# Kernel tuning notes

Hardware: AMD Instinct MI355X
Metric: run time of the kernel (lower is better)

Reference implementation:

```python
import jax, jax.numpy as jnp
import numpy as np
import math

B, L, H, NH = 4, 2048, 2048, 16
HD = H // NH  # head_dim = 128
ROPE_BASE = 10000.0


def rotate_half(x):
    x1, x2 = jnp.split(x, 2, axis=-1)
    return jnp.concatenate((-x2, x1), axis=-1)


def rope_cos_sin(seq_len, dim, dtype=jnp.float32):
    inv_freq = 1.0 / (ROPE_BASE ** (jnp.arange(0, dim, 2, dtype=jnp.float32) / dim))
    t = jnp.arange(seq_len, dtype=jnp.float32)
    freqs = jnp.outer(t, inv_freq)              # [L, dim/2]
    emb = jnp.concatenate((freqs, freqs), -1)   # [L, dim]
    return jnp.cos(emb).astype(dtype), jnp.sin(emb).astype(dtype)


def setup_inputs() -> dict:
    key = jax.random.key(0)
    ks = jax.random.split(key, 5)
    x = jax.random.normal(ks[0], (B, L, H), dtype=jnp.float32)
    # causal mask, broadcastable over [B, NH, L, L]; 0 -> masked
    mask = jnp.tril(jnp.ones((L, L), dtype=jnp.int32))[None, None]
    s = 0.02
    Wq = jax.random.normal(ks[1], (H, H), dtype=jnp.float32) * s
    Wk = jax.random.normal(ks[2], (H, H), dtype=jnp.float32) * s
    Wv = jax.random.normal(ks[3], (H, H), dtype=jnp.float32) * s
    Wo = jax.random.normal(ks[4], (H, H), dtype=jnp.float32) * s
    return {"x": x, "mask": mask, "Wq": Wq, "Wk": Wk, "Wv": Wv, "Wo": Wo}


def reference(x, mask, Wq, Wk, Wv, Wo):
    b, l, _ = x.shape
    # nn.Linear: y = x @ W.T (weight shape [out, in])
    q = (x @ Wq.T).reshape(b, l, NH, HD).transpose(0, 2, 1, 3)  # [B,H,L,D]
    k = (x @ Wk.T).reshape(b, l, NH, HD).transpose(0, 2, 1, 3)
    v = (x @ Wv.T).reshape(b, l, NH, HD).transpose(0, 2, 1, 3)
    cos, sin = rope_cos_sin(l, HD, x.dtype)  # [L, D] broadcasts over [B,H,L,D]
    q = q * cos + rotate_half(q) * sin
    k = k * cos + rotate_half(k) * sin
    attn = jnp.einsum("bhqd,bhkd->bhqk", q, k) / math.sqrt(HD)
    attn = jnp.where(mask == 0, jnp.float32(-jnp.inf), attn)
    attn = jax.nn.softmax(attn.astype(jnp.float32), axis=-1).astype(x.dtype)
    out = jnp.einsum("bhqk,bhkd->bhqd", attn, v)
    out = out.transpose(0, 2, 1, 3).reshape(b, l, NH * HD)
    return out @ Wo.T
```

## Files before the change

### kernel.cpp

```cpp
#include <hip/hip_runtime.h>
#include <cstdint>
#include <cmath>

#define B_   4
#define L_   2048
#define H_   2048
#define NH_  16
#define HD_  128
#define ML_  (B_*L_)

using short8 = __attribute__((ext_vector_type(8))) short;
using f32x4  = __attribute__((ext_vector_type(4))) float;
using f32x16 = __attribute__((ext_vector_type(16))) float;
using uint4v = __attribute__((ext_vector_type(4))) unsigned;

__device__ inline short f2bf(float f){
  unsigned u = __builtin_bit_cast(unsigned, f);
  unsigned r = u + 0x7FFFu + ((u >> 16) & 1u);
  return (short)(r >> 16);
}
__device__ inline float bf2f(short s){
  unsigned u = ((unsigned)(unsigned short)s) << 16;
  return __builtin_bit_cast(float, u);
}

#define GLD16(gp, lp) __builtin_amdgcn_global_load_lds(                      \
    (const __attribute__((address_space(1))) void*)(gp),                     \
    (__attribute__((address_space(3))) void*)(lp), 16, 0, 0)

__device__ inline unsigned cvtpk_bf16(float lo, float hi){
  unsigned d;
  asm("v_cvt_pk_bf16_f32 %0, %1, %2" : "=v"(d) : "v"(lo), "v"(hi));
  return d;
}
__device__ inline void permswap32(unsigned &a, unsigned &b){
  asm volatile("v_permlane32_swap_b32 %0, %1" : "+v"(a), "+v"(b));
}
__device__ inline float cross_half_max(float x){
  return fmaxf(x, __shfl_xor(x, 32));
}
__device__ inline float cross_half_add(float x){
  return x + __shfl_xor(x, 32);
}

__global__ void rope_table(float* __restrict__ cosT, float* __restrict__ sinT){
  int idx = blockIdx.x * 256 + threadIdx.x;
  if (idx >= L_ * 64) return;
  int l = idx >> 6, d = idx & 63;
  float invf = powf(10000.0f, -(float)d * (1.0f/64.0f));
  float fr = (float)l * invf;
  cosT[idx] = cosf(fr);
  sinT[idx] = sinf(fr);
}

__global__ __launch_bounds__(256)
void cvt_bf16(const float* __restrict__ in, short* __restrict__ out, int n8){
  int i = blockIdx.x * 256 + threadIdx.x;
  if (i >= n8) return;
  const float4* p = (const float4*)(in + (size_t)i * 8);
  float4 a = p[0], b = p[1];
  short8 s;
  s[0]=f2bf(a.x); s[1]=f2bf(a.y); s[2]=f2bf(a.z); s[3]=f2bf(a.w);
  s[4]=f2bf(b.x); s[5]=f2bf(b.y); s[6]=f2bf(b.z); s[7]=f2bf(b.w);
  *(short8*)(out + (size_t)i * 8) = s;
}

__global__ __launch_bounds__(256)
void cvt_w3(const float* __restrict__ W0, const float* __restrict__ W1,
            const float* __restrict__ W2, short* __restrict__ out){
  int i = blockIdx.x * 256 + threadIdx.x;
  const int per = H_ * H_ / 8;
  const float* src; int j;
  if (i < per)            { src = W0; j = i; }
  else if (i < 2 * per)   { src = W1; j = i - per; }
  else                    { src = W2; j = i - 2 * per; }
  const float4* p = (const float4*)(src + (size_t)j * 8);
  float4 a = p[0], b = p[1];
  short8 s;
  s[0]=f2bf(a.x); s[1]=f2bf(a.y); s[2]=f2bf(a.z); s[3]=f2bf(a.w);
  s[4]=f2bf(b.x); s[5]=f2bf(b.y); s[6]=f2bf(b.z); s[7]=f2bf(b.w);
  *(short8*)(out + (size_t)i * 8) = s;
}

template<int QKV, int OUT_F32>
__global__ __launch_bounds__(512, 2)
void gemm256_bt(const short* __restrict__ A, const short* __restrict__ Bw,
                void* __restrict__ C0, void* __restrict__ C1,
                void* __restrict__ C2)
{
  constexpr int K = 2048, N = 2048;
  __shared__ short sA[4][256 * 32];
  __shared__ short sB[4][256 * 32];
  const int tid  = threadIdx.x;
  const int lane = tid & 63;
  const int wave = tid >> 6;
  const int wr = wave >> 2, wc = wave & 3;
  const int ln = lane & 15, g = lane >> 4;

  const int blk = blockIdx.x;
  int n_t, m_t;
  if constexpr (QKV) { int i = blk >> 3; n_t = (blk & 7) + 8 * (i >> 5); m_t = i & 31; }
  else               { n_t = blk & 7;    m_t = blk >> 3; }
  const int m0 = m_t * 256;
  const int nb0 = n_t * 256;

  const int u0 = wave * 64 + lane;
  const int u1 = u0 + 512;
  const int r0 = u0 >> 2, c0 = (((u0 & 3) ^ (r0 & 3) ^ ((r0 >> 2) & 3))) * 8;
  const int r1 = u1 >> 2, c1 = (((u1 & 3) ^ (r1 & 3) ^ ((r1 >> 2) & 3))) * 8;

  f32x4 acc[8][4];
  #pragma unroll
  for (int m = 0; m < 8; m++)
    #pragma unroll
    for (int n = 0; n < 4; n++) acc[m][n] = {0.f, 0.f, 0.f, 0.f};

#define STAGE256(T) do {                                                     \
    const int _b = (T) & 3; const int _k = (T) * 32;                         \
    GLD16(A  + (size_t)(m0 + r0) * K + _k + c0, &sA[_b][wave * 512]);        \
    GLD16(A  + (size_t)(m0 + r1) * K + _k + c1, &sA[_b][4096 + wave * 512]); \
    GLD16(Bw + (size_t)(nb0 + r0) * K + _k + c0, &sB[_b][wave * 512]);       \
    GLD16(Bw + (size_t)(nb0 + r1) * K + _k + c1, &sB[_b][4096 + wave * 512]);\
  } while (0)

#define TILE256(T, VMN, PF) do {                                             \
    asm volatile("s_waitcnt vmcnt(" #VMN ")" ::: "memory");                  \
    __builtin_amdgcn_s_barrier();                                            \
    asm volatile("" ::: "memory");                                           \
    const short* _at = &sA[(T) & 3][0];                                      \
    const short* _bt = &sB[(T) & 3][0];                                      \
    short8 af[8], bfr[4];                                                    \
    const int _sl = (g ^ (ln & 3) ^ ((ln >> 2) & 3)) * 8;                    \
    _Pragma("unroll")                                                        \
    for (int m = 0; m < 8; m++)                                              \
      af[m] = *(const short8*)(_at + (wr * 128 + m * 16 + ln) * 32 + _sl);   \
    _Pragma("unroll")                                                        \
    for (int n = 0; n < 4; n++)                                              \
      bfr[n] = *(const short8*)(_bt + (wc * 64 + n * 16 + ln) * 32 + _sl);   \
    if (PF) STAGE256((T) + 3);                                               \
    __builtin_amdgcn_s_setprio(1);                                           \
    _Pragma("unroll")                                                        \
    for (int m = 0; m < 8; m++)                                              \
      _Pragma("unroll")                                                      \
      for (int n = 0; n < 4; n++)                                            \
        acc[m][n] = __builtin_amdgcn_mfma_f32_16x16x32_bf16(af[m], bfr[n],   \
                                                            acc[m][n], 0, 0, 0); \
    __builtin_amdgcn_s_setprio(0);                                           \
  } while (0)

  STAGE256(0); STAGE256(1); STAGE256(2);

  for (int t = 0; t < 61; ++t) TILE256(t, 8, true);
  TILE256(61, 8, false);
  TILE256(62, 4, false);
  TILE256(63, 0, false);

#undef STAGE256
#undef TILE256

  void* Cp; int cb;
  if constexpr (QKV) {
    int w = n_t >> 3;
    Cp = (w == 0) ? C0 : (w == 1) ? C1 : C2;
    cb = (n_t & 7) * 256;
  } else { Cp = C0; cb = nb0; }
  #pragma unroll
  for (int m = 0; m < 8; m++)
    #pragma unroll
    for (int n = 0; n < 4; n++)
      #pragma unroll
      for (int r = 0; r < 4; r++) {
        int row = m0 + wr * 128 + m * 16 + g * 4 + r;
        int col = cb + wc * 64 + n * 16 + ln;
        float v = acc[m][n][r];
        if constexpr (OUT_F32) ((float*)Cp)[(size_t)row * N + col] = v;
        else                   ((short*)Cp)[(size_t)row * N + col] = f2bf(v);
      }
}

__global__ __launch_bounds__(256)
void rope_apply_k(short* __restrict__ Kb,
                  const float* __restrict__ cosT, const float* __restrict__ sinT)
{
  int idx = blockIdx.x * 256 + threadIdx.x;
  int row = idx >> 7;
  int rem = idx & 127;
  int h = rem >> 3, ch = rem & 7;
  int l = row & (L_ - 1);
  short* base = Kb + (size_t)row * H_ + h * HD_ + ch * 8;
  short8 lo = *(short8*)base;
  short8 hi = *(short8*)(base + 64);
  const float* cp = cosT + l * 64 + ch * 8;
  const float* sp = sinT + l * 64 + ch * 8;
  short8 nlo, nhi;
  #pragma unroll
  for (int j = 0; j < 8; j++) {
    float c = cp[j], s = sp[j];
    float x0 = bf2f(lo[j]), x1 = bf2f(hi[j]);
    nlo[j] = f2bf(x0 * c - x1 * s);
    nhi[j] = f2bf(x1 * c + x0 * s);
  }
  *(short8*)base        = nlo;
  *(short8*)(base + 64) = nhi;
}

__global__ __launch_bounds__(256)
void transpose_v(const short* __restrict__ Vb, short* __restrict__ VT)
{
  __shared__ short t[64 * 64];
  const int blk = blockIdx.x;
  const int dt = blk & 1, lt = (blk >> 1) & 31, bh = blk >> 6;
  const int b = bh >> 4, h = bh & 15;
  const int l0 = lt * 64, d0 = dt * 64;
  const int tid = threadIdx.x;
  #pragma unroll
  for (int i = 0; i < 2; i++) {
    int u = tid + i * 256;
    int r = u >> 3, c = u & 7;
    short8 v = *(const short8*)(Vb + ((size_t)b * L_ + l0 + r) * H_ + h * HD_ + d0 + c * 8);
    *(short8*)&t[r * 64 + ((c ^ ((r >> 3) & 7)) << 3)] = v;
  }
  __syncthreads();
  #pragma unroll
  for (int i = 0; i < 2; i++) {
    int u = tid + i * 256;
    int d = u >> 3, lc = u & 7;
    short8 o;
    #pragma unroll
    for (int j = 0; j < 8; j++) {
      int l = lc * 8 + j;
      o[j] = t[l * 64 + (((d >> 3) ^ (lc & 7)) << 3) + (d & 7)];
    }
    *(short8*)(VT + ((size_t)bh * HD_ + d0 + d) * L_ + l0 + lc * 8) = o;
  }
}

__global__ __launch_bounds__(512, 2)
void flash_attn(const short* __restrict__ Qb, const short* __restrict__ Kb,
                const short* __restrict__ VT, short* __restrict__ AO,
                const float* __restrict__ cosT, const float* __restrict__ sinT)
{
  __shared__ short lds_k[2][64 * 128];
  __shared__ short lds_v[2][128 * 64];
  __shared__ float f_lds[8][32];

  const int blk = blockIdx.x;
  int bh, j;
  if (blk < 256) { bh = blk & 63; j = 7 - (blk >> 6); }
  else           { int u = blk - 256; bh = u & 63; j = 3 - (u >> 6); }
  const int q0 = j * 256;
  const int T  = 4 * j + 4;
  const int h = bh & 15, b = bh >> 4;
  const int tid = threadIdx.x, wave = tid >> 6, lane = tid & 63;
  const int hi = lane >> 5, l31 = lane & 31;
  const size_t rowbase = (size_t)b * L_;
  const int colbase = h * HD_;
  const short* Kbh  = Kb + rowbase * H_ + colbase;
  const short* VTbh = VT + (size_t)bh * HD_ * L_;
  const int qw = q0 + wave * 32;
  const int qabs = qw + l31;
  const int fsw = (l31 & 7) ^ ((l31 >> 3) & 3);

  short8 qf[8];
  {
    const short* qp = Qb + (rowbase + qabs) * H_ + colbase + hi * 8;
    short8 qraw[8];
    #pragma unroll
    for (int c = 0; c < 8; c++) qraw[c] = *(const short8*)(qp + c * 16);
    const int lq = qabs & (L_ - 1);
    const float* cp = cosT + lq * 64 + hi * 8;
    const float* sp = sinT + lq * 64 + hi * 8;
    #pragma unroll
    for (int c = 0; c < 4; c++) {
      #pragma unroll
      for (int jj = 0; jj < 8; jj++) {
        float cc = cp[c * 16 + jj], ss = sp[c * 16 + jj];
        float lo = bf2f(qraw[c][jj]), hv = bf2f(qraw[c + 4][jj]);
        qf[c][jj]     = f2bf((lo * cc - hv * ss) * 0.08838834764831845f);
        qf[c + 4][jj] = f2bf((hv * cc + lo * ss) * 0.08838834764831845f);
      }
    }
  }

  f32x16 acc_o[4];
  #pragma unroll
  for (int d = 0; d < 4; d++)
    #pragma unroll
    for (int r = 0; r < 16; r++) acc_o[d][r] = 0.f;
  float m_ = -__builtin_inff(), l_ = 0.f;

  auto stage = [&](int k0s, int bufi) {
    #pragma unroll
    for (int i = 0; i < 2; i++) {
      int c = wave * 2 + i;
      {
        int rt = c * 4 + (lane >> 4);
        int cg = (lane & 15) ^ (rt & 7) ^ ((rt >> 3) & 3);
        const short* gp = Kbh + (size_t)(k0s + rt) * H_ + cg * 8;
        GLD16(gp, &lds_k[bufi][c * 512]);
      }
      {
        int rd = c * 8 + (lane >> 3);
        int cg = (lane & 7) ^ (rd & 7) ^ ((rd >> 3) & 3);
        const short* gp = VTbh + (size_t)rd * L_ + k0s + cg * 8;
        GLD16(gp, &lds_v[bufi][c * 512]);
      }
    }
  };

  stage(0, 0);
  __syncthreads();

  for (int t = 0; t < T; ++t) {
    const int k0 = t * 64;
    if (t + 1 < T) stage((t + 1) * 64, (t + 1) & 1);
    const short* kb_ = lds_k[t & 1];
    const short* vb_ = lds_v[t & 1];

    if (k0 <= qw + 31) {
      f32x16 p0, p1;
      #pragma unroll
      for (int r = 0; r < 16; r++) { p0[r] = 0.f; p1[r] = 0.f; }
      __builtin_amdgcn_s_setprio(1);
      #pragma unroll
      for (int c = 0; c < 8; c++) {
        int ch = (c * 2 + hi) ^ fsw;
        short8 kf0 = *(const short8*)(kb_ + l31 * 128 + ch * 8);
        short8 kf1 = *(const short8*)(kb_ + (32 + l31) * 128 + ch * 8);
        p0 = __builtin_amdgcn_mfma_f32_32x32x16_bf16(kf0, qf[c], p0, 0, 0, 0);
        p1 = __builtin_amdgcn_mfma_f32_32x32x16_bf16(kf1, qf[c], p1, 0, 0, 0);
      }
      __builtin_amdgcn_s_setprio(0);

      if (k0 + 63 > qw) {
        #pragma unroll
        for (int r = 0; r < 16; r++) {
          int kvl = (r & 3) + 8 * (r >> 2) + 4 * hi;
          if (k0 + kvl > qabs)      p0[r] = -__builtin_inff();
          if (k0 + 32 + kvl > qabs) p1[r] = -__builtin_inff();
        }
      }

      float mt = p0[0];
      #pragma unroll
      for (int r = 1; r < 16; r++) mt = fmaxf(mt, p0[r]);
      #pragma unroll
      for (int r = 0; r < 16; r++) mt = fmaxf(mt, p1[r]);
      mt = cross_half_max(mt);
      if (!__all(mt <= m_ + 8.0f)) {
        float mnew = fmaxf(m_, mt);
        float f = __expf(m_ - mnew);
        m_ = mnew;
        l_ *= f;
        if (lane < 32) f_lds[wave][lane] = f;
        f32x4 fr[4];
        #pragma unroll
        for (int i = 0; i < 4; i++)
          fr[i] = *(const f32x4*)&f_lds[wave][i * 8 + hi * 4];
        #pragma unroll
        for (int d = 0; d < 4; d++)
          #pragma unroll
          for (int r = 0; r < 16; r++) acc_o[d][r] *= fr[r >> 2][r & 3];
      }
      float ls = 0.f;
      #pragma unroll
      for (int r = 0; r < 16; r++) { p0[r] = __expf(p0[r] - m_); ls += p0[r]; }
      #pragma unroll
      for (int r = 0; r < 16; r++) { p1[r] = __expf(p1[r] - m_); ls += p1[r]; }
      ls = cross_half_add(ls);
      l_ += ls;

      __builtin_amdgcn_s_setprio(1);
      #pragma unroll
      for (int ks = 0; ks < 4; ks++) {
        const f32x16 &pp = (ks < 2) ? p0 : p1;
        const int kk = (ks & 1) * 8;
        unsigned a0 = cvtpk_bf16(pp[kk + 0], pp[kk + 1]);
        unsigned b0 = cvtpk_bf16(pp[kk + 4], pp[kk + 5]);
        permswap32(a0, b0);
        unsigned a1 = cvtpk_bf16(pp[kk + 2], pp[kk + 3]);
        unsigned b1 = cvtpk_bf16(pp[kk + 6], pp[kk + 7]);
        permswap32(a1, b1);
        uint4v w; w[0] = a0; w[1] = a1; w[2] = b0; w[3] = b1;
        short8 af = __builtin_bit_cast(short8, w);
        #pragma unroll
        for (int db = 0; db < 4; db++) {
          int d  = db * 32 + l31;
          int ch = (ks * 2 + hi) ^ fsw;
          short8 vf = *(const short8*)(vb_ + d * 64 + ch * 8);
          acc_o[db] = __builtin_amdgcn_mfma_f32_32x32x16_bf16(af, vf, acc_o[db], 0, 0, 0);
        }
      }
      __builtin_amdgcn_s_setprio(0);
    }
    __syncthreads();
  }

  if (lane < 32) f_lds[wave][lane] = 1.0f / l_;
  f32x4 lr[4];
  #pragma unroll
  for (int i = 0; i < 4; i++)
    lr[i] = *(const f32x4*)&f_lds[wave][i * 8 + hi * 4];
  #pragma unroll
  for (int db = 0; db < 4; db++)
    #pragma unroll
    for (int r = 0; r < 16; r++) {
      int row = qw + (r & 3) + 8 * (r >> 2) + 4 * hi;
      AO[(rowbase + row) * H_ + colbase + db * 32 + l31] =
          f2bf(acc_o[db][r] * lr[r >> 2][r & 3]);
    }
}

extern "C" void kernel_launch(void* const* d_in, const int* in_sizes, int n_in,
                              void* d_out, int out_size, void* d_ws, size_t ws_size,
                              hipStream_t stream)
{
  const float* x  = (const float*)d_in[0];
  const float* Wq = (const float*)d_in[2];
  const float* Wk = (const float*)d_in[3];
  const float* Wv = (const float*)d_in[4];
  const float* Wo = (const float*)d_in[5];
  float* out = (float*)d_out;

  char* ws = (char*)d_ws;
  const size_t SZ = (size_t)ML_ * H_ * sizeof(short);
  short* Qb = (short*)(ws);
  short* Kb = (short*)(ws + SZ);
  short* Vb = (short*)(ws + 2 * SZ);
  short* xb = (short*)(ws + 3 * SZ);
  short* VT = xb;
  short* AO = Vb;
  float* cosT = (float*)(ws + 4 * SZ);
  float* sinT = cosT + (size_t)L_ * 64;
  short* Wb = (short*)(ws + 4 * SZ + (size_t)(1 << 20));
  const size_t NEED_FUSED = 4 * SZ + (1 << 20) + (size_t)3 * H_ * H_ * sizeof(short);
  const bool fused = ws_size >= NEED_FUSED;

  rope_table<<<512, 256, 0, stream>>>(cosT, sinT);

  cvt_bf16<<<ML_ * H_ / 8 / 256, 256, 0, stream>>>(x, xb, ML_ * H_ / 8);

  if (fused) {
    cvt_w3<<<3 * H_ * H_ / 8 / 256, 256, 0, stream>>>(Wq, Wk, Wv, Wb);
    gemm256_bt<1, 0><<<768, 512, 0, stream>>>(xb, Wb, Qb, Kb, Vb);
  } else {
    cvt_bf16<<<H_ * H_ / 8 / 256, 256, 0, stream>>>(Wq, Wb, H_ * H_ / 8);
    gemm256_bt<0, 0><<<256, 512, 0, stream>>>(xb, Wb, Qb, Qb, Qb);
    cvt_bf16<<<H_ * H_ / 8 / 256, 256, 0, stream>>>(Wk, Wb, H_ * H_ / 8);
    gemm256_bt<0, 0><<<256, 512, 0, stream>>>(xb, Wb, Kb, Kb, Kb);
    cvt_bf16<<<H_ * H_ / 8 / 256, 256, 0, stream>>>(Wv, Wb, H_ * H_ / 8);
    gemm256_bt<0, 0><<<256, 512, 0, stream>>>(xb, Wb, Vb, Vb, Vb);
  }

  transpose_v<<<64 * 32 * 2, 256, 0, stream>>>(Vb, VT);

  rope_apply_k<<<ML_ * NH_ * 8 / 256, 256, 0, stream>>>(Kb, cosT, sinT);

  flash_attn<<<512, 512, 0, stream>>>(Qb, Kb, VT, AO, cosT, sinT);

  cvt_bf16<<<H_ * H_ / 8 / 256, 256, 0, stream>>>(Wo, Wb, H_ * H_ / 8);
  gemm256_bt<0, 1><<<256, 512, 0, stream>>>(AO, Wb, out, out, out);
}
```

Baseline: 446.0 us.

## Shrink GEMM tiles to 128x128 and merge prep/post kernels into fewer launches

The GEMM drops from 256x256 tiles with 512 threads to 128x128 tiles with 256 threads. The grid grows from 256 to 1024 blocks per 2048x2048 projection, which gives more parallelism across CUs. The rope table, x/weight conversions and the Wo conversion are merged into one prep kernel, and the V transpose and K rope into one post_qkv kernel, to cut launch count. Smaller tiles reduce operand reuse and raise global/L2 traffic per FLOP.

```diff
diff --git a/kernel.cpp b/kernel.cpp
--- a/kernel.cpp
+++ b/kernel.cpp
@@ -41,6 +41,16 @@
 }
 __device__ inline float cross_half_add(float x){
   return x + __shfl_xor(x, 32);
+}
+
+__device__ inline void cvt8(const float* __restrict__ in, short* __restrict__ out,
+                            int i){
+  const float4* p = (const float4*)(in + (size_t)i * 8);
+  float4 a = p[0], b = p[1];
+  short8 s;
+  s[0]=f2bf(a.x); s[1]=f2bf(a.y); s[2]=f2bf(a.z); s[3]=f2bf(a.w);
+  s[4]=f2bf(b.x); s[5]=f2bf(b.y); s[6]=f2bf(b.z); s[7]=f2bf(b.w);
+  *(short8*)(out + (size_t)i * 8) = s;
 }
 
 __global__ void rope_table(float* __restrict__ cosT, float* __restrict__ sinT){
@@ -57,90 +67,103 @@
 void cvt_bf16(const float* __restrict__ in, short* __restrict__ out, int n8){
   int i = blockIdx.x * 256 + threadIdx.x;
   if (i >= n8) return;
-  const float4* p = (const float4*)(in + (size_t)i * 8);
-  float4 a = p[0], b = p[1];
-  short8 s;
-  s[0]=f2bf(a.x); s[1]=f2bf(a.y); s[2]=f2bf(a.z); s[3]=f2bf(a.w);
-  s[4]=f2bf(b.x); s[5]=f2bf(b.y); s[6]=f2bf(b.z); s[7]=f2bf(b.w);
-  *(short8*)(out + (size_t)i * 8) = s;
+  cvt8(in, out, i);
 }
 
 __global__ __launch_bounds__(256)
-void cvt_w3(const float* __restrict__ W0, const float* __restrict__ W1,
-            const float* __restrict__ W2, short* __restrict__ out){
-  int i = blockIdx.x * 256 + threadIdx.x;
+void prep(const float* __restrict__ x,  const float* __restrict__ Wq,
+          const float* __restrict__ Wk, const float* __restrict__ Wv,
+          const float* __restrict__ Wo, short* __restrict__ xb,
+          short* __restrict__ Wb, short* __restrict__ WoB,
+          float* __restrict__ cosT, float* __restrict__ sinT)
+{
+  const int blk = blockIdx.x, tid = threadIdx.x;
   const int per = H_ * H_ / 8;
-  const float* src; int j;
-  if (i < per)            { src = W0; j = i; }
-  else if (i < 2 * per)   { src = W1; j = i - per; }
-  else                    { src = W2; j = i - 2 * per; }
-  const float4* p = (const float4*)(src + (size_t)j * 8);
-  float4 a = p[0], b = p[1];
-  short8 s;
-  s[0]=f2bf(a.x); s[1]=f2bf(a.y); s[2]=f2bf(a.z); s[3]=f2bf(a.w);
-  s[4]=f2bf(b.x); s[5]=f2bf(b.y); s[6]=f2bf(b.z); s[7]=f2bf(b.w);
-  *(short8*)(out + (size_t)i * 8) = s;
+  if (blk < 8192) {
+    cvt8(x, xb, blk * 256 + tid);
+  } else if (blk < 14336) {
+    int i = (blk - 8192) * 256 + tid;
+    const float* src; int j;
+    if (i < per)          { src = Wq; j = i; }
+    else if (i < 2 * per) { src = Wk; j = i - per; }
+    else                  { src = Wv; j = i - 2 * per; }
+    const float4* p = (const float4*)(src + (size_t)j * 8);
+    float4 a = p[0], b = p[1];
+    short8 s;
+    s[0]=f2bf(a.x); s[1]=f2bf(a.y); s[2]=f2bf(a.z); s[3]=f2bf(a.w);
+    s[4]=f2bf(b.x); s[5]=f2bf(b.y); s[6]=f2bf(b.z); s[7]=f2bf(b.w);
+    *(short8*)(Wb + (size_t)i * 8) = s;
+  } else if (blk < 16384) {
+    cvt8(Wo, WoB, (blk - 14336) * 256 + tid);
+  } else {
+    int idx = (blk - 16384) * 256 + tid;
+    int l = idx >> 6, d = idx & 63;
+    float invf = powf(10000.0f, -(float)d * (1.0f/64.0f));
+    float fr = (float)l * invf;
+    cosT[idx] = cosf(fr);
+    sinT[idx] = sinf(fr);
+  }
 }
 
 template<int QKV, int OUT_F32>
-__global__ __launch_bounds__(512, 2)
-void gemm256_bt(const short* __restrict__ A, const short* __restrict__ Bw,
+__global__ __launch_bounds__(256, 2)
+void gemm128_bt(const short* __restrict__ A, const short* __restrict__ Bw,
                 void* __restrict__ C0, void* __restrict__ C1,
                 void* __restrict__ C2)
 {
   constexpr int K = 2048, N = 2048;
-  __shared__ short sA[4][256 * 32];
-  __shared__ short sB[4][256 * 32];
+  __shared__ short sA[4][128 * 32];
+  __shared__ short sB[4][128 * 32];
   const int tid  = threadIdx.x;
   const int lane = tid & 63;
   const int wave = tid >> 6;
-  const int wr = wave >> 2, wc = wave & 3;
+  const int wr = wave >> 1, wc = wave & 1;
   const int ln = lane & 15, g = lane >> 4;
 
   const int blk = blockIdx.x;
-  int n_t, m_t;
-  if constexpr (QKV) { int i = blk >> 3; n_t = (blk & 7) + 8 * (i >> 5); m_t = i & 31; }
-  else               { n_t = blk & 7;    m_t = blk >> 3; }
-  const int m0 = m_t * 256;
-  const int nb0 = n_t * 256;
-
-  const int u0 = wave * 64 + lane;
-  const int u1 = u0 + 512;
+  const int i = blk >> 3;
+  const int n_t = (blk & 7) + 8 * (i >> 6);
+  const int m_t = i & 63;
+  const int m0 = m_t * 128;
+  const int nb0 = n_t * 128;
+
+  const int u0 = tid;
+  const int u1 = tid + 256;
   const int r0 = u0 >> 2, c0 = (((u0 & 3) ^ (r0 & 3) ^ ((r0 >> 2) & 3))) * 8;
   const int r1 = u1 >> 2, c1 = (((u1 & 3) ^ (r1 & 3) ^ ((r1 >> 2) & 3))) * 8;
 
-  f32x4 acc[8][4];
+  f32x4 acc[4][4];
   #pragma unroll
-  for (int m = 0; m < 8; m++)
+  for (int m = 0; m < 4; m++)
     #pragma unroll
     for (int n = 0; n < 4; n++) acc[m][n] = {0.f, 0.f, 0.f, 0.f};
 
-#define STAGE256(T) do {                                                     \
+#define STAGE128(T) do {                                                     \
     const int _b = (T) & 3; const int _k = (T) * 32;                         \
     GLD16(A  + (size_t)(m0 + r0) * K + _k + c0, &sA[_b][wave * 512]);        \
-    GLD16(A  + (size_t)(m0 + r1) * K + _k + c1, &sA[_b][4096 + wave * 512]); \
+    GLD16(A  + (size_t)(m0 + r1) * K + _k + c1, &sA[_b][2048 + wave * 512]); \
     GLD16(Bw + (size_t)(nb0 + r0) * K + _k + c0, &sB[_b][wave * 512]);       \
-    GLD16(Bw + (size_t)(nb0 + r1) * K + _k + c1, &sB[_b][4096 + wave * 512]);\
+    GLD16(Bw + (size_t)(nb0 + r1) * K + _k + c1, &sB[_b][2048 + wave * 512]);\
   } while (0)
 
-#define TILE256(T, VMN, PF) do {                                             \
+#define TILE128(T, VMN, PF) do {                                             \
     asm volatile("s_waitcnt vmcnt(" #VMN ")" ::: "memory");                  \
     __builtin_amdgcn_s_barrier();                                            \
     asm volatile("" ::: "memory");                                           \
     const short* _at = &sA[(T) & 3][0];                                      \
     const short* _bt = &sB[(T) & 3][0];                                      \
-    short8 af[8], bfr[4];                                                    \
+    short8 af[4], bfr[4];                                                    \
     const int _sl = (g ^ (ln & 3) ^ ((ln >> 2) & 3)) * 8;                    \
     _Pragma("unroll")                                                        \
-    for (int m = 0; m < 8; m++)                                              \
-      af[m] = *(const short8*)(_at + (wr * 128 + m * 16 + ln) * 32 + _sl);   \
+    for (int m = 0; m < 4; m++)                                              \
+      af[m] = *(const short8*)(_at + (wr * 64 + m * 16 + ln) * 32 + _sl);    \
     _Pragma("unroll")                                                        \
     for (int n = 0; n < 4; n++)                                              \
       bfr[n] = *(const short8*)(_bt + (wc * 64 + n * 16 + ln) * 32 + _sl);   \
-    if (PF) STAGE256((T) + 3);                                               \
+    if (PF) STAGE128((T) + 3);                                               \
     __builtin_amdgcn_s_setprio(1);                                           \
     _Pragma("unroll")                                                        \
-    for (int m = 0; m < 8; m++)                                              \
+    for (int m = 0; m < 4; m++)                                              \
       _Pragma("unroll")                                                      \
       for (int n = 0; n < 4; n++)                                            \
         acc[m][n] = __builtin_amdgcn_mfma_f32_16x16x32_bf16(af[m], bfr[n],   \
@@ -148,29 +171,29 @@
     __builtin_amdgcn_s_setprio(0);                                           \
   } while (0)
 
-  STAGE256(0); STAGE256(1); STAGE256(2);
-
-  for (int t = 0; t < 61; ++t) TILE256(t, 8, true);
-  TILE256(61, 8, false);
-  TILE256(62, 4, false);
-  TILE256(63, 0, false);
-
-#undef STAGE256
-#undef TILE256
+  STAGE128(0); STAGE128(1); STAGE128(2);
+
+  for (int t = 0; t < 61; ++t) TILE128(t, 8, true);
+  TILE128(61, 8, false);
+  TILE128(62, 4, false);
+  TILE128(63, 0, false);
+
+#undef STAGE128
+#undef TILE128
 
   void* Cp; int cb;
   if constexpr (QKV) {
-    int w = n_t >> 3;
+    int w = n_t >> 4;
     Cp = (w == 0) ? C0 : (w == 1) ? C1 : C2;
-    cb = (n_t & 7) * 256;
+    cb = (n_t & 15) * 128;
   } else { Cp = C0; cb = nb0; }
   #pragma unroll
-  for (int m = 0; m < 8; m++)
+  for (int m = 0; m < 4; m++)
     #pragma unroll
     for (int n = 0; n < 4; n++)
       #pragma unroll
       for (int r = 0; r < 4; r++) {
-        int row = m0 + wr * 128 + m * 16 + g * 4 + r;
+        int row = m0 + wr * 64 + m * 16 + g * 4 + r;
         int col = cb + wc * 64 + n * 16 + ln;
         float v = acc[m][n][r];
         if constexpr (OUT_F32) ((float*)Cp)[(size_t)row * N + col] = v;
@@ -179,59 +202,58 @@
 }
 
 __global__ __launch_bounds__(256)
-void rope_apply_k(short* __restrict__ Kb,
-                  const float* __restrict__ cosT, const float* __restrict__ sinT)
-{
-  int idx = blockIdx.x * 256 + threadIdx.x;
-  int row = idx >> 7;
-  int rem = idx & 127;
-  int h = rem >> 3, ch = rem & 7;
-  int l = row & (L_ - 1);
-  short* base = Kb + (size_t)row * H_ + h * HD_ + ch * 8;
-  short8 lo = *(short8*)base;
-  short8 hi = *(short8*)(base + 64);
-  const float* cp = cosT + l * 64 + ch * 8;
-  const float* sp = sinT + l * 64 + ch * 8;
-  short8 nlo, nhi;
-  #pragma unroll
-  for (int j = 0; j < 8; j++) {
-    float c = cp[j], s = sp[j];
-    float x0 = bf2f(lo[j]), x1 = bf2f(hi[j]);
-    nlo[j] = f2bf(x0 * c - x1 * s);
-    nhi[j] = f2bf(x1 * c + x0 * s);
-  }
-  *(short8*)base        = nlo;
-  *(short8*)(base + 64) = nhi;
-}
-
-__global__ __launch_bounds__(256)
-void transpose_v(const short* __restrict__ Vb, short* __restrict__ VT)
+void post_qkv(const short* __restrict__ Vb, short* __restrict__ VT,
+              short* __restrict__ Kb,
+              const float* __restrict__ cosT, const float* __restrict__ sinT)
 {
   __shared__ short t[64 * 64];
-  const int blk = blockIdx.x;
-  const int dt = blk & 1, lt = (blk >> 1) & 31, bh = blk >> 6;
-  const int b = bh >> 4, h = bh & 15;
-  const int l0 = lt * 64, d0 = dt * 64;
   const int tid = threadIdx.x;
-  #pragma unroll
-  for (int i = 0; i < 2; i++) {
-    int u = tid + i * 256;
-    int r = u >> 3, c = u & 7;
-    short8 v = *(const short8*)(Vb + ((size_t)b * L_ + l0 + r) * H_ + h * HD_ + d0 + c * 8);
-    *(short8*)&t[r * 64 + ((c ^ ((r >> 3) & 7)) << 3)] = v;
-  }
-  __syncthreads();
-  #pragma unroll
-  for (int i = 0; i < 2; i++) {
-    int u = tid + i * 256;
-    int d = u >> 3, lc = u & 7;
-    short8 o;
+  if (blockIdx.x < 4096) {
+    const int blk = blockIdx.x;
+    const int dt = blk & 1, lt = (blk >> 1) & 31, bh = blk >> 6;
+    const int b = bh >> 4, h = bh & 15;
+    const int l0 = lt * 64, d0 = dt * 64;
+    #pragma unroll
+    for (int i = 0; i < 2; i++) {
+      int u = tid + i * 256;
+      int r = u >> 3, c = u & 7;
+      short8 v = *(const short8*)(Vb + ((size_t)b * L_ + l0 + r) * H_ + h * HD_ + d0 + c * 8);
+      *(short8*)&t[r * 64 + ((c ^ ((r >> 3) & 7)) << 3)] = v;
+    }
+    __syncthreads();
+    #pragma unroll
+    for (int i = 0; i < 2; i++) {
+      int u = tid + i * 256;
+      int d = u >> 3, lc = u & 7;
+      short8 o;
+      #pragma unroll
+      for (int j = 0; j < 8; j++) {
+        int l = lc * 8 + j;
+        o[j] = t[l * 64 + (((d >> 3) ^ (lc & 7)) << 3) + (d & 7)];
+      }
+      *(short8*)(VT + ((size_t)bh * HD_ + d0 + d) * L_ + l0 + lc * 8) = o;
+    }
+  } else {
+    int idx = (blockIdx.x - 4096) * 256 + tid;
+    int row = idx >> 7;
+    int rem = idx & 127;
+    int h = rem >> 3, ch = rem & 7;
+    int l = row & (L_ - 1);
+    short* base = Kb + (size_t)row * H_ + h * HD_ + ch * 8;
+    short8 lo = *(short8*)base;
+    short8 hi = *(short8*)(base + 64);
+    const float* cp = cosT + l * 64 + ch * 8;
+    const float* sp = sinT + l * 64 + ch * 8;
+    short8 nlo, nhi;
     #pragma unroll
     for (int j = 0; j < 8; j++) {
-      int l = lc * 8 + j;
-      o[j] = t[l * 64 + (((d >> 3) ^ (lc & 7)) << 3) + (d & 7)];
-    }
-    *(short8*)(VT + ((size_t)bh * HD_ + d0 + d) * L_ + l0 + lc * 8) = o;
+      float c = cp[j], s = sp[j];
+      float x0 = bf2f(lo[j]), x1 = bf2f(hi[j]);
+      nlo[j] = f2bf(x0 * c - x1 * s);
+      nhi[j] = f2bf(x1 * c + x0 * s);
+    }
+    *(short8*)base        = nlo;
+    *(short8*)(base + 64) = nhi;
   }
 }
 
@@ -432,32 +454,29 @@
   short* AO = Vb;
   float* cosT = (float*)(ws + 4 * SZ);
   float* sinT = cosT + (size_t)L_ * 64;
-  short* Wb = (short*)(ws + 4 * SZ + (size_t)(1 << 20));
-  const size_t NEED_FUSED = 4 * SZ + (1 << 20) + (size_t)3 * H_ * H_ * sizeof(short);
+  short* Wb  = (short*)(ws + 4 * SZ + (size_t)(1 << 20));
+  short* WoB = Wb + (size_t)3 * H_ * H_;
+  const size_t NEED_FUSED = 4 * SZ + (1 << 20) + (size_t)4 * H_ * H_ * sizeof(short);
   const bool fused = ws_size >= NEED_FUSED;
 
-  rope_table<<<512, 256, 0, stream>>>(cosT, sinT);
-
-  cvt_bf16<<<ML_ * H_ / 8 / 256, 256, 0, stream>>>(x, xb, ML_ * H_ / 8);
-
   if (fused) {
-    cvt_w3<<<3 * H_ * H_ / 8 / 256, 256, 0, stream>>>(Wq, Wk, Wv, Wb);
-    gemm256_bt<1, 0><<<768, 512, 0, stream>>>(xb, Wb, Qb, Kb, Vb);
+    prep<<<16896, 256, 0, stream>>>(x, Wq, Wk, Wv, Wo, xb, Wb, WoB, cosT, sinT);
+    gemm128_bt<1, 0><<<3072, 256, 0, stream>>>(xb, Wb, Qb, Kb, Vb);
+    post_qkv<<<8192, 256, 0, stream>>>(Vb, VT, Kb, cosT, sinT);
+    flash_attn<<<512, 512, 0, stream>>>(Qb, Kb, VT, AO, cosT, sinT);
+    gemm128_bt<0, 1><<<1024, 256, 0, stream>>>(AO, WoB, out, out, out);
   } else {
+    rope_table<<<512, 256, 0, stream>>>(cosT, sinT);
+    cvt_bf16<<<ML_ * H_ / 8 / 256, 256, 0, stream>>>(x, xb, ML_ * H_ / 8);
     cvt_bf16<<<H_ * H_ / 8 / 256, 256, 0, stream>>>(Wq, Wb, H_ * H_ / 8);
-    gemm256_bt<0, 0><<<256, 512, 0, stream>>>(xb, Wb, Qb, Qb, Qb);
+    gemm128_bt<0, 0><<<1024, 256, 0, stream>>>(xb, Wb, Qb, Qb, Qb);
     cvt_bf16<<<H_ * H_ / 8 / 256, 256, 0, stream>>>(Wk, Wb, H_ * H_ / 8);
-    gemm256_bt<0, 0><<<256, 512, 0, stream>>>(xb, Wb, Kb, Kb, Kb);
+    gemm128_bt<0, 0><<<1024, 256, 0, stream>>>(xb, Wb, Kb, Kb, Kb);
     cvt_bf16<<<H_ * H_ / 8 / 256, 256, 0, stream>>>(Wv, Wb, H_ * H_ / 8);
-    gemm256_bt<0, 0><<<256, 512, 0, stream>>>(xb, Wb, Vb, Vb, Vb);
+    gemm128_bt<0, 0><<<1024, 256, 0, stream>>>(xb, Wb, Vb, Vb, Vb);
+    post_qkv<<<8192, 256, 0, stream>>>(Vb, VT, Kb, cosT, sinT);
+    flash_attn<<<512, 512, 0, stream>>>(Qb, Kb, VT, AO, cosT, sinT);
+    cvt_bf16<<<H_ * H_ / 8 / 256, 256, 0, stream>>>(Wo, Wb, H_ * H_ / 8);
+    gemm128_bt<0, 1><<<1024, 256, 0, stream>>>(AO, Wb, out, out, out);
   }
-
-  transpose_v<<<64 * 32 * 2, 256, 0, stream>>>(Vb, VT);
-
-  rope_apply_k<<<ML_ * NH_ * 8 / 256, 256, 0, stream>>>(Kb, cosT, sinT);
-
-  flash_attn<<<512, 512, 0, stream>>>(Qb, Kb, VT, AO, cosT, sinT);
-
-  cvt_bf16<<<H_ * H_ / 8 / 256, 256, 0, stream>>>(Wo, Wb, H_ * H_ / 8);
-  gemm256_bt<0, 1><<<256, 512, 0, stream>>>(AO, Wb, out, out, out);
-}
+}
```

New measurement: 515.3 us. +15.6%, slower.
